# Kernel optimization log

Hardware: AMD Instinct MI355X
Metric: run time of the kernel (lower is better)

The kernel has to match this reference:

```python
import jax, jax.numpy as jnp
import numpy as np

P = 16
IMG_SIZES = [(512, 512), (512, 384), (448, 512), (384, 384), (320, 448), (256, 512), (384, 256), (512, 320)]
LMAX = 1024
B, DIM, HEADS, DH, DEPTH, MLP, NC = 8, 512, 8, 64, 6, 2048, 1000
PD = 3 * P * P  # 768 patch dim


def layer_norm(x, w, b=None, eps=1e-5):
    mu = x.mean(-1, keepdims=True)
    var = ((x - mu) ** 2).mean(-1, keepdims=True)
    y = (x - mu) * jax.lax.rsqrt(var + eps) * w
    return y + b if b is not None else y


def _pack(images):
    # slice each image to its true (static) resolution, patchify, pad to LMAX
    toks, his, wis, msks = [], [], [], []
    for i, (H, W) in enumerate(IMG_SIZES):
        h, w = H // P, W // P
        L = h * w
        img = images[i, :, :H, :W]
        t = img.reshape(3, h, P, w, P).transpose(1, 3, 0, 2, 4).reshape(L, PD)
        hi = jnp.repeat(jnp.arange(h), w)
        wi = jnp.tile(jnp.arange(w), h)
        pad = LMAX - L
        toks.append(jnp.pad(t, ((0, pad), (0, 0))))
        his.append(jnp.pad(hi, (0, pad)))
        wis.append(jnp.pad(wi, (0, pad)))
        msks.append(jnp.arange(LMAX) < L)
    return jnp.stack(toks), jnp.stack(his), jnp.stack(wis), jnp.stack(msks)


def _mha(qx, kx, kmask, wq, wk, wv, qn, kn, wo):
    Bq, Lq, _ = qx.shape
    Lk = kx.shape[1]
    q = (qx @ wq.T).reshape(Bq, Lq, HEADS, DH)
    k = (kx @ wk.T).reshape(Bq, Lk, HEADS, DH)
    v = (kx @ wv.T).reshape(Bq, Lk, HEADS, DH)
    q = layer_norm(q, qn)
    k = layer_norm(k, kn)
    s = jnp.einsum('bqhd,bkhd->bhqk', q, k) / np.sqrt(DH).astype(np.float32)
    s = s + jnp.where(kmask[:, None, None, :], 0.0, -1e9)
    a = jax.nn.softmax(s, axis=-1)
    o = jnp.einsum('bhqk,bkhd->bqhd', a, v).reshape(Bq, Lq, HEADS * DH)
    return o @ wo.T


def setup_inputs() -> dict:
    key = jax.random.key(0)
    ks = iter(jax.random.split(key, 48))

    def nrm(shape, s=0.02):
        return jax.random.normal(next(ks), shape, jnp.float32) * s

    return {
        'images': jax.random.normal(next(ks), (B, 3, 512, 512), jnp.float32),
        'pe_ln1_w': jnp.ones(PD), 'pe_ln1_b': jnp.zeros(PD),
        'pe_w': nrm((DIM, PD)), 'pe_b': jnp.zeros(DIM),
        'pe_ln2_w': jnp.ones(DIM), 'pe_ln2_b': jnp.zeros(DIM),
        'pos_h': nrm((32, DIM), 1.0), 'pos_w': nrm((32, DIM), 1.0),
        'attn_ln': jnp.ones((DEPTH, DIM)),
        'wq': nrm((DEPTH, DIM, DIM)), 'wk': nrm((DEPTH, DIM, DIM)), 'wv': nrm((DEPTH, DIM, DIM)),
        'qn': jnp.ones((DEPTH, DH)), 'kn': jnp.ones((DEPTH, DH)),
        'wo': nrm((DEPTH, DIM, DIM)),
        'ff_ln': jnp.ones((DEPTH, DIM)),
        'ff_w1': nrm((DEPTH, MLP, DIM)), 'ff_b1': jnp.zeros((DEPTH, MLP)),
        'ff_w2': nrm((DEPTH, DIM, MLP)), 'ff_b2': jnp.zeros((DEPTH, DIM)),
        'final_ln': jnp.ones(DIM),
        'pool_q': nrm((DIM,), 1.0), 'pool_ln': jnp.ones(DIM),
        'pool_wq': nrm((DIM, DIM)), 'pool_wk': nrm((DIM, DIM)), 'pool_wv': nrm((DIM, DIM)),
        'pool_qn': jnp.ones(DH), 'pool_kn': jnp.ones(DH),
        'pool_wo': nrm((DIM, DIM)),
        'head_ln': jnp.ones(DIM), 'head_w': nrm((NC, DIM)),
    }


def reference(images, pe_ln1_w, pe_ln1_b, pe_w, pe_b, pe_ln2_w, pe_ln2_b, pos_h, pos_w,
              attn_ln, wq, wk, wv, qn, kn, wo, ff_ln, ff_w1, ff_b1, ff_w2, ff_b2,
              final_ln, pool_q, pool_ln, pool_wq, pool_wk, pool_wv, pool_qn, pool_kn,
              pool_wo, head_ln, head_w):
    tok, hi, wi, mask = _pack(images)
    t = layer_norm(tok, pe_ln1_w, pe_ln1_b)
    t = t @ pe_w.T + pe_b
    t = layer_norm(t, pe_ln2_w, pe_ln2_b)
    t = t + pos_h[hi] + pos_w[wi]
    t = t * mask[..., None]
    for l in range(DEPTH):
        xn = layer_norm(t, attn_ln[l])
        t = t + _mha(xn, xn, mask, wq[l], wk[l], wv[l], qn[l], kn[l], wo[l])
        h = layer_norm(t, ff_ln[l])
        t = t + (jax.nn.gelu(h @ ff_w1[l].T + ff_b1[l], approximate=False) @ ff_w2[l].T + ff_b2[l])
    t = layer_norm(t, final_ln)
    # attention pooling: one learned query per image; context = transformer output (unnormed inside attn)
    q = jnp.broadcast_to(pool_q, (B, 1, DIM))
    qn_ = layer_norm(q, pool_ln)
    pooled = _mha(qn_, t, mask, pool_wq, pool_wk, pool_wv, pool_qn, pool_kn, pool_wo)[:, 0]
    return layer_norm(pooled, head_ln) @ head_w.T
```

## Files before the change

kernel.cpp:

```cpp
#include <hip/hip_runtime.h>
#include <math.h>

#define LMAXS 1024
#define NB 8
#define DIM 512
#define HEADS 8
#define DH 64
#define DEPTH 6
#define MLP 2048
#define NC 1000
#define PDIM 768
#define MPACK 5376
#define MVALID 5360
#define QSCALE 0.18033688f

typedef __attribute__((ext_vector_type(8))) short short8;
typedef __attribute__((ext_vector_type(4))) float floatx4;
typedef unsigned short ushort;

__constant__ int c_w[8]   = {32,24,32,24,28,32,16,20};
__constant__ int c_L[8]   = {1024,768,896,576,560,512,384,640};
__constant__ int c_off[9] = {0,1024,1792,2688,3264,3824,4336,4720,5360};

__device__ __forceinline__ int row2img(int r) {
  int b = 0;
  #pragma unroll
  for (int i = 1; i < 8; ++i) if (r >= c_off[i]) b = i;
  return b;
}

__device__ __forceinline__ ushort f2bf(float x) {
  unsigned int u = __float_as_uint(x);
  u += 0x7fff + ((u >> 16) & 1);
  return (ushort)(u >> 16);
}

#define GLOAD_LDS16(gp, lp) \
  __builtin_amdgcn_global_load_lds((const __attribute__((address_space(1))) void*)(gp), \
                                   (__attribute__((address_space(3))) void*)(lp), 16, 0, 0)

__device__ __forceinline__ void reduce2_256(float& s, float& s2, float* red) {
  #pragma unroll
  for (int off = 32; off; off >>= 1) {
    s  += __shfl_xor(s, off);
    s2 += __shfl_xor(s2, off);
  }
  int wv = threadIdx.x >> 6;
  if ((threadIdx.x & 63) == 0) { red[wv*2] = s; red[wv*2+1] = s2; }
  __syncthreads();
  s  = red[0] + red[2] + red[4] + red[6];
  s2 = red[1] + red[3] + red[5] + red[7];
  __syncthreads();
}

__global__ __launch_bounds__(256) void cvt_k(const float* __restrict__ s, ushort* __restrict__ d, int n) {
  int i = blockIdx.x*256 + threadIdx.x;
  if (i < n) d[i] = f2bf(s[i]);
}
__global__ __launch_bounds__(256) void cvt_qkv_k(
    const float* __restrict__ wq, const float* __restrict__ wk, const float* __restrict__ wv,
    ushort* __restrict__ d) {
  int i = blockIdx.x*256 + threadIdx.x;
  if (i >= 6*1536*512) return;
  int l = i / (1536*512), r = (i / 512) % 1536, k = i & 511;
  const float* src = (r < 512) ? wq : (r < 1024) ? wk : wv;
  int rr = r & 511;
  d[i] = f2bf(src[(size_t)l*DIM*DIM + (size_t)rr*DIM + k]);
}
__global__ __launch_bounds__(256) void cvt_pool_k(
    const float* __restrict__ wk, const float* __restrict__ wv, ushort* __restrict__ d) {
  int i = blockIdx.x*256 + threadIdx.x;
  if (i >= 1024*512) return;
  int r = i >> 9, k = i & 511;
  d[i] = f2bf(r < 512 ? wk[(size_t)r*DIM + k] : wv[(size_t)(r-512)*DIM + k]);
}

__global__ __launch_bounds__(256) void pack_ln1_k(
    const float* __restrict__ images, const float* __restrict__ g,
    const float* __restrict__ bb, ushort* __restrict__ tok) {
  int r = blockIdx.x;
  ushort* out = tok + (size_t)r * PDIM;
  if (r >= MVALID) {
    for (int i = threadIdx.x; i < PDIM; i += 256) out[i] = 0;
    return;
  }
  int b = row2img(r), l = r - c_off[b];
  int wgrid = c_w[b];
  __shared__ float vals[PDIM];
  __shared__ float red[8];
  int hp = l / wgrid, wp = l % wgrid;
  const float* base = images + (size_t)b*3*512*512 + (size_t)hp*16*512 + wp*16;
  float s = 0.f, s2 = 0.f;
  for (int i = threadIdx.x; i < PDIM; i += 256) {
    int c = i >> 8, rr = (i >> 4) & 15, cc = i & 15;
    float v = base[(size_t)c*512*512 + rr*512 + cc];
    vals[i] = v; s += v; s2 += v*v;
  }
  reduce2_256(s, s2, red);
  float mu = s * (1.f/PDIM);
  float rs = rsqrtf(fmaxf(s2*(1.f/PDIM) - mu*mu, 0.f) + 1e-5f);
  for (int i = threadIdx.x; i < PDIM; i += 256)
    out[i] = f2bf((vals[i]-mu)*rs*g[i] + bb[i]);
}

template<int TM, int TN, int WM, int WN, int ACT, int OUT>
__global__ __launch_bounds__(256) void gemm_t(
    const ushort* __restrict__ A, const ushort* __restrict__ W,
    const float* __restrict__ bias, void* __restrict__ Cv,
    int M, int N, int K) {
  constexpr int WAVES_N = TN / WN;
  constexpr int FM = WM / 16, FN = WN / 16;
  constexpr int NA = TM / 32, NW = TN / 32;
  __shared__ ushort As[TM*64];
  __shared__ ushort Ws[TN*64];
  int tid = threadIdx.x;
  int row0 = blockIdx.y*TM, col0 = blockIdx.x*TN;
  int lane = tid & 63, l15 = lane & 15, quad = lane >> 4;
  int wv = tid >> 6;
  int wm = wv / WAVES_N, wn = wv % WAVES_N;
  int sw = l15 & 7;
  int segA = (quad ^ sw) * 8, segB = segA ^ 32;
  const ushort *Ap[NA], *Wp[NW];
  #pragma unroll
  for (int j = 0; j < NA; ++j) {
    int blk = j*256 + tid;
    int r = blk >> 3, s = ((blk & 7) ^ (r & 7)) * 8;
    Ap[j] = A + (size_t)(row0 + r)*K + s;
  }
  #pragma unroll
  for (int j = 0; j < NW; ++j) {
    int blk = j*256 + tid;
    int r = blk >> 3, s = ((blk & 7) ^ (r & 7)) * 8;
    Wp[j] = W + (size_t)(col0 + r)*K + s;
  }
  floatx4 acc[FM][FN] = {};
  for (int k0 = 0; k0 < K; k0 += 64) {
    __syncthreads();
    #pragma unroll
    for (int j = 0; j < NA; ++j) GLOAD_LDS16(Ap[j] + k0, &As[(j*256+tid)*8]);
    #pragma unroll
    for (int j = 0; j < NW; ++j) GLOAD_LDS16(Wp[j] + k0, &Ws[(j*256+tid)*8]);
    __syncthreads();
    #pragma unroll
    for (int w = 0; w < 2; ++w) {
      int sg = w ? segB : segA;
      short8 af[FM], bf[FN];
      #pragma unroll
      for (int i = 0; i < FM; ++i) af[i] = *(const short8*)&As[(wm*WM + i*16 + l15)*64 + sg];
      #pragma unroll
      for (int j = 0; j < FN; ++j) bf[j] = *(const short8*)&Ws[(wn*WN + j*16 + l15)*64 + sg];
      #pragma unroll
      for (int i = 0; i < FM; ++i)
        #pragma unroll
        for (int j = 0; j < FN; ++j)
          acc[i][j] = __builtin_amdgcn_mfma_f32_16x16x32_bf16(af[i], bf[j], acc[i][j], 0, 0, 0);
    }
  }
  int rb = row0 + wm*WM + quad*4;
  int cb = col0 + wn*WN + l15;
  #pragma unroll
  for (int j = 0; j < FN; ++j) {
    int cc = cb + j*16;
    float bsum = bias ? bias[cc] : 0.f;
    #pragma unroll
    for (int i = 0; i < FM; ++i) {
      int rr = rb + i*16;
      #pragma unroll
      for (int reg = 0; reg < 4; ++reg) {
        float v = acc[i][j][reg] + bsum;
        if (ACT == 1) v = 0.5f*v*(1.f + erff(v*0.70710678118654752f));
        size_t idx = (size_t)(rr + reg)*N + cc;
        if (OUT == 0)      ((float*)Cv)[idx] = v;
        else if (OUT == 1) ((float*)Cv)[idx] += v;
        else               ((ushort*)Cv)[idx] = f2bf(v);
      }
    }
  }
}

template<int POOL>
__global__ __launch_bounds__(256) void gemm_qkv_k(
    const ushort* __restrict__ A, const ushort* __restrict__ W,
    const float* __restrict__ gq, const float* __restrict__ gk,
    ushort* __restrict__ Qh, ushort* __restrict__ Kh, ushort* __restrict__ Vh,
    float* __restrict__ KV, int N) {
  const int K = DIM;
  __shared__ ushort As[128*64];
  __shared__ ushort Ws[128*64];
  int tid = threadIdx.x;
  int row0 = blockIdx.y*128, col0 = blockIdx.x*128;
  int lane = tid & 63, l15 = lane & 15, quad = lane >> 4;
  int wv = tid >> 6, wm = wv >> 1, wn = wv & 1;
  int sw = l15 & 7;
  int segA = (quad ^ sw) * 8, segB = segA ^ 32;
  const ushort *Ap[4], *Wp[4];
  #pragma unroll
  for (int j = 0; j < 4; ++j) {
    int blk = j*256 + tid;
    int r = blk >> 3, s = ((blk & 7) ^ (r & 7)) * 8;
    Ap[j] = A + (size_t)(row0 + r)*K + s;
    Wp[j] = W + (size_t)(col0 + r)*K + s;
  }
  floatx4 acc[4][4] = {};
  for (int k0 = 0; k0 < K; k0 += 64) {
    __syncthreads();
    #pragma unroll
    for (int j = 0; j < 4; ++j) {
      GLOAD_LDS16(Ap[j] + k0, &As[(j*256+tid)*8]);
      GLOAD_LDS16(Wp[j] + k0, &Ws[(j*256+tid)*8]);
    }
    __syncthreads();
    #pragma unroll
    for (int w = 0; w < 2; ++w) {
      int sg = w ? segB : segA;
      short8 af[4], bf[4];
      #pragma unroll
      for (int i = 0; i < 4; ++i) af[i] = *(const short8*)&As[(wm*64 + i*16 + l15)*64 + sg];
      #pragma unroll
      for (int j = 0; j < 4; ++j) bf[j] = *(const short8*)&Ws[(wn*64 + j*16 + l15)*64 + sg];
      #pragma unroll
      for (int i = 0; i < 4; ++i)
        #pragma unroll
        for (int j = 0; j < 4; ++j)
          acc[i][j] = __builtin_amdgcn_mfma_f32_16x16x32_bf16(af[i], bf[j], acc[i][j], 0, 0, 0);
    }
  }
  int unit = (col0 >> 6) + wn;
  bool needln = POOL ? (unit < 8) : (unit < 16);
  const float* gain = POOL ? gq : (unit < 8 ? gq : gk);
  #pragma unroll
  for (int i = 0; i < 4; ++i) {
    float s[4] = {0,0,0,0}, s2[4] = {0,0,0,0};
    if (needln) {
      #pragma unroll
      for (int j = 0; j < 4; ++j)
        #pragma unroll
        for (int reg = 0; reg < 4; ++reg) {
          float v = acc[i][j][reg];
          s[reg] += v; s2[reg] += v*v;
        }
      #pragma unroll
      for (int reg = 0; reg < 4; ++reg)
        #pragma unroll
        for (int off = 1; off < 16; off <<= 1) {
          s[reg]  += __shfl_xor(s[reg],  off);
          s2[reg] += __shfl_xor(s2[reg], off);
        }
    }
    #pragma unroll
    for (int reg = 0; reg < 4; ++reg) {
      int r = row0 + wm*64 + i*16 + quad*4 + reg;
      if (r >= MVALID) continue;
      float mu = s[reg]*(1.f/64.f);
      float rs = rsqrtf(fmaxf(s2[reg]*(1.f/64.f) - mu*mu, 0.f) + 1e-5f);
      int b = row2img(r), l = r - c_off[b];
      #pragma unroll
      for (int j = 0; j < 4; ++j) {
        int dh = j*16 + l15;
        float v = acc[i][j][reg];
        if (needln) v = (v - mu)*rs*gain[dh];
        if (POOL) {
          KV[(size_t)r*1024 + unit*64 + dh] = v;
        } else {
          int h = unit & 7;
          size_t dst = ((size_t)(b*8+h)*LMAXS + l)*64 + dh;
          if (unit < 8)       Qh[dst] = f2bf(v * QSCALE);
          else if (unit < 16) Kh[dst] = f2bf(v);
          else                Vh[dst] = f2bf(v);
        }
      }
    }
  }
}

__global__ __launch_bounds__(256) void row_ln_bf_k(
    const float* __restrict__ T, const float* __restrict__ g, ushort* __restrict__ Y) {
  __shared__ float red[8];
  size_t base = (size_t)blockIdx.x * DIM;
  float v0 = T[base + threadIdx.x], v1 = T[base + threadIdx.x + 256];
  float s = v0 + v1, s2 = v0*v0 + v1*v1;
  reduce2_256(s, s2, red);
  float mu = s*(1.f/DIM), rs = rsqrtf(fmaxf(s2*(1.f/DIM) - mu*mu, 0.f) + 1e-5f);
  Y[base + threadIdx.x]       = f2bf((v0-mu)*rs*g[threadIdx.x]);
  Y[base + threadIdx.x + 256] = f2bf((v1-mu)*rs*g[threadIdx.x + 256]);
}

__global__ __launch_bounds__(256) void ln2_pos_k(
    float* __restrict__ T, const float* __restrict__ g, const float* __restrict__ bb,
    const float* __restrict__ ph, const float* __restrict__ pw) {
  int r = blockIdx.x;
  float* x = T + (size_t)r * DIM;
  if (r >= MVALID) {
    for (int i = threadIdx.x; i < DIM; i += 256) x[i] = 0.f;
    return;
  }
  int b = row2img(r), l = r - c_off[b];
  __shared__ float red[8];
  int wgrid = c_w[b];
  int hi = l / wgrid, wi = l % wgrid;
  float s=0.f, s2=0.f;
  for (int i = threadIdx.x; i < DIM; i += 256) { float v = x[i]; s+=v; s2+=v*v; }
  reduce2_256(s, s2, red);
  float mu = s*(1.f/DIM), rs = rsqrtf(fmaxf(s2*(1.f/DIM)-mu*mu, 0.f)+1e-5f);
  for (int i = threadIdx.x; i < DIM; i += 256)
    x[i] = (x[i]-mu)*rs*g[i] + bb[i] + ph[hi*DIM+i] + pw[wi*DIM+i];
}

__global__ __launch_bounds__(256) void vtrans_k(
    const ushort* __restrict__ Vh, ushort* __restrict__ VhT) {
  int bh = blockIdx.x, b = bh >> 3;
  int Lb = c_L[b];
  int lt = blockIdx.y;
  if (lt*64 >= Lb) return;
  __shared__ ushort t[64][72];
  int tid = threadIdx.x;
  int row = tid >> 2, seg = (tid & 3)*16;
  short8 z8 = {};
  if (lt*64 + row < Lb) {
    const ushort* src = Vh + ((size_t)bh*LMAXS + lt*64 + row)*64 + seg;
    *(short8*)&t[row][seg]   = *(const short8*)src;
    *(short8*)&t[row][seg+8] = *(const short8*)(src+8);
  } else {
    *(short8*)&t[row][seg]   = z8;
    *(short8*)&t[row][seg+8] = z8;
  }
  __syncthreads();
  int dh = tid >> 2, ks = (tid & 3)*16;
  short8 o0, o1;
  #pragma unroll
  for (int jj = 0; jj < 8; ++jj) o0[jj] = (short)t[ks+jj][dh];
  #pragma unroll
  for (int jj = 0; jj < 8; ++jj) o1[jj] = (short)t[ks+8+jj][dh];
  ushort* dst = VhT + ((size_t)bh*64 + dh)*LMAXS + lt*64 + ks;
  *(short8*)dst     = o0;
  *(short8*)(dst+8) = o1;
}

__global__ __launch_bounds__(256) void attn_part_k(
    const ushort* __restrict__ Qh, const ushort* __restrict__ Kh,
    const ushort* __restrict__ VhT, float* __restrict__ PART) {
  int bh = blockIdx.x, b = bh >> 3;
  int Lb = c_L[b];
  int qt = blockIdx.y, z = blockIdx.z;
  if (qt*64 >= Lb || z*512 >= Lb) return;
  __shared__ ushort Ks[64*64];
  __shared__ ushort Vt[64*64];
  __shared__ ushort Pb[4][16][68];
  int tid = threadIdx.x, wv = tid >> 6, lane = tid & 63;
  int quad = lane >> 4, l15 = lane & 15;
  int sw = l15 & 7;
  int segA = (quad ^ sw) * 8, segB = segA ^ 32;
  int q0 = qt*64 + wv*16;
  bool active = q0 < Lb;
  const ushort* qhb = Qh + (size_t)bh * LMAXS * DH;
  const ushort* khb = Kh + (size_t)bh * LMAXS * DH;
  const ushort* vtb = VhT + (size_t)bh * DH * LMAXS;
  short8 aq0 = {}, aq1 = {};
  if (active) {
    const ushort* qp = qhb + (size_t)(q0 + l15) * DH;
    aq0 = *(const short8*)(qp + quad*8);
    aq1 = *(const short8*)(qp + 32 + quad*8);
  }
  int blk0 = tid, blk1 = tid + 256;
  int kr0 = blk0 >> 3, s0 = ((blk0 & 7) ^ (kr0 & 7)) * 8;
  int kr1 = blk1 >> 3, s1 = ((blk1 & 7) ^ (kr1 & 7)) * 8;
  const ushort* kg0 = khb + kr0*DH + s0;
  const ushort* kg1 = khb + kr1*DH + s1;
  const ushort* vg0 = vtb + (size_t)kr0*LMAXS + s0;
  const ushort* vg1 = vtb + (size_t)kr1*LMAXS + s1;
  int kbeg = z*512, kend = min(kbeg + 512, Lb);
  float lsum[4] = {0.f,0.f,0.f,0.f};
  floatx4 o[4] = {};
  for (int kc = kbeg; kc < kend; kc += 64) {
    __syncthreads();
    GLOAD_LDS16(kg0 + kc*DH, &Ks[blk0*8]);
    GLOAD_LDS16(kg1 + kc*DH, &Ks[blk1*8]);
    GLOAD_LDS16(vg0 + kc,    &Vt[blk0*8]);
    GLOAD_LDS16(vg1 + kc,    &Vt[blk1*8]);
    __syncthreads();
    if (!active) continue;
    bool tail = (kc + 64 > Lb);
    #pragma unroll
    for (int kb = 0; kb < 4; ++kb) {
      int krow = (kb*16 + l15) * 64;
      floatx4 s = {};
      s = __builtin_amdgcn_mfma_f32_16x16x32_bf16(aq0, *(const short8*)&Ks[krow + segA], s, 0,0,0);
      s = __builtin_amdgcn_mfma_f32_16x16x32_bf16(aq1, *(const short8*)&Ks[krow + segB], s, 0,0,0);
      #pragma unroll
      for (int reg = 0; reg < 4; ++reg) {
        float x = s[reg];
        if (tail && (kc + kb*16 + l15 >= Lb)) x = -1e9f;
        float p = __builtin_amdgcn_exp2f(x);
        lsum[reg] += p;
        Pb[wv][quad*4+reg][kb*16+l15] = f2bf(p);
      }
    }
    short8 a0 = *(const short8*)&Pb[wv][l15][quad*8];
    short8 a1 = *(const short8*)&Pb[wv][l15][32+quad*8];
    #pragma unroll
    for (int nb = 0; nb < 4; ++nb) {
      int vrow = (nb*16 + l15) * 64;
      o[nb] = __builtin_amdgcn_mfma_f32_16x16x32_bf16(a0, *(const short8*)&Vt[vrow + segA], o[nb], 0,0,0);
      o[nb] = __builtin_amdgcn_mfma_f32_16x16x32_bf16(a1, *(const short8*)&Vt[vrow + segB], o[nb], 0,0,0);
    }
  }
  if (active) {
    size_t sb = ((size_t)(bh*16 + qt)*2 + z) * 4160;
    #pragma unroll
    for (int reg = 0; reg < 4; ++reg) {
      float s = lsum[reg];
      s += __shfl_xor(s,1); s += __shfl_xor(s,2); s += __shfl_xor(s,4); s += __shfl_xor(s,8);
      if (l15 == 0) PART[sb + 4096 + wv*16 + quad*4 + reg] = s;
    }
    int rq = wv*16 + quad*4;
    #pragma unroll
    for (int nb = 0; nb < 4; ++nb)
      #pragma unroll
      for (int reg = 0; reg < 4; ++reg)
        PART[sb + (size_t)(rq + reg)*64 + nb*16 + l15] = o[nb][reg];
  }
}

__global__ __launch_bounds__(256) void attn_comb_k(
    const float* __restrict__ PART, ushort* __restrict__ O) {
  int bh = blockIdx.x, b = bh >> 3, h = bh & 7;
  int Lb = c_L[b];
  int qt = blockIdx.y;
  if (qt*64 >= Lb) return;
  int nsl = (Lb + 511) >> 9;
  int t = threadIdx.x;
  int q = t >> 2, dj = (t & 3) * 16;
  int qq = qt*64 + q;
  if (qq >= Lb) return;
  size_t base = (size_t)(bh*16 + qt)*2*4160;
  float o[16] = {};
  float l = 0.f;
  for (int zz = 0; zz < nsl; ++zz) {
    const float* sp = PART + base + (size_t)zz*4160;
    #pragma unroll
    for (int i = 0; i < 16; i += 4) {
      float4 v = *(const float4*)&sp[q*64 + dj + i];
      o[i] += v.x; o[i+1] += v.y; o[i+2] += v.z; o[i+3] += v.w;
    }
    l += sp[4096 + q];
  }
  float inv = 1.f / l;
  short8 r0, r1;
  #pragma unroll
  for (int i = 0; i < 8; ++i) r0[i] = (short)f2bf(o[i]*inv);
  #pragma unroll
  for (int i = 0; i < 8; ++i) r1[i] = (short)f2bf(o[8+i]*inv);
  ushort* dst = O + (size_t)(c_off[b]+qq)*DIM + h*DH + dj;
  *(short8*)dst     = r0;
  *(short8*)(dst+8) = r1;
}

__global__ __launch_bounds__(256) void pool_prep_a_k(
    const float* __restrict__ pq, const float* __restrict__ pln,
    const float* __restrict__ pwq, float* __restrict__ qp) {
  __shared__ float qln[DIM];
  __shared__ float red[8];
  int tid = threadIdx.x;
  float s=0.f, s2=0.f;
  for (int i=tid;i<DIM;i+=256){ float v=pq[i]; s+=v; s2+=v*v; }
  reduce2_256(s, s2, red);
  float mu=s*(1.f/DIM), rs=rsqrtf(fmaxf(s2*(1.f/DIM)-mu*mu,0.f)+1e-5f);
  for (int i=tid;i<DIM;i+=256) qln[i]=(pq[i]-mu)*rs*pln[i];
  __syncthreads();
  int n = blockIdx.x*64 + (tid>>2);
  int kq = (tid&3)*128;
  const float4* wr = (const float4*)(pwq + (size_t)n*DIM + kq);
  float a=0.f;
  #pragma unroll
  for (int k=0;k<32;++k) {
    float4 w4 = wr[k];
    float4 q4 = *(const float4*)&qln[kq + k*4];
    a += w4.x*q4.x + w4.y*q4.y + w4.z*q4.z + w4.w*q4.w;
  }
  a += __shfl_xor(a,1); a += __shfl_xor(a,2);
  if ((tid&3)==0) qp[n]=a;
}

__global__ __launch_bounds__(512) void pool_prep_b_k(
    const float* __restrict__ qp, const float* __restrict__ pqn, float* __restrict__ qpool) {
  int h = threadIdx.x >> 6, lane = threadIdx.x & 63;
  float v = qp[h*64 + lane];
  float s = v, s2 = v*v;
  #pragma unroll
  for (int off=32; off; off>>=1) { s += __shfl_xor(s,off); s2 += __shfl_xor(s2,off); }
  float mu = s*(1.f/64), rs = rsqrtf(fmaxf(s2*(1.f/64)-mu*mu, 0.f)+1e-5f);
  qpool[h*64+lane] = (v-mu)*rs*pqn[lane];
}

__global__ __launch_bounds__(256) void pool_attn_part_k(
    const float* __restrict__ qpool, const float* __restrict__ KV,
    float* __restrict__ PARTP) {
  __shared__ float qh[DH];
  __shared__ float ps[256];
  __shared__ float op[4][DH];
  __shared__ float red[8];
  int bh = blockIdx.x, c = blockIdx.y;
  int b = bh>>3, h = bh&7;
  int Lb = c_L[b];
  int tid = threadIdx.x;
  if (tid < DH) qh[tid] = qpool[h*DH + tid];
  __syncthreads();
  int kk = c*256 + tid;
  float p = 0.f;
  if (kk < Lb) {
    const float4* kp = (const float4*)(KV + (size_t)(c_off[b]+kk)*1024 + h*DH);
    float a = 0.f;
    #pragma unroll
    for (int dd=0; dd<16; ++dd) {
      float4 kv = kp[dd];
      a += kv.x*qh[dd*4] + kv.y*qh[dd*4+1] + kv.z*qh[dd*4+2] + kv.w*qh[dd*4+3];
    }
    p = __expf(a*0.125f);
  }
  ps[tid] = p;
  float s = p, s2 = 0.f;
  reduce2_256(s, s2, red);
  int wvv = tid >> 6, lane = tid & 63;
  float o = 0.f;
  int kb = c*256 + wvv*64;
  const float* vb = KV + (size_t)c_off[b]*1024 + 512 + h*DH + lane;
  for (int j = 0; j < 64; ++j) {
    int key = kb + j;
    if (key < Lb) o += ps[wvv*64+j] * vb[(size_t)key*1024];
  }
  op[wvv][lane] = o;
  __syncthreads();
  if (tid < DH)
    PARTP[((size_t)bh*4 + c)*66 + tid] = op[0][tid]+op[1][tid]+op[2][tid]+op[3][tid];
  if (tid == 64)
    PARTP[((size_t)bh*4 + c)*66 + 64] = s;
}

__global__ __launch_bounds__(64) void pool_attn_comb_k(
    const float* __restrict__ PARTP, float* __restrict__ O) {
  int bh = blockIdx.x, b = bh>>3, h = bh&7, d = threadIdx.x;
  float o = 0.f, sum = 0.f;
  #pragma unroll
  for (int c = 0; c < 4; ++c) {
    o   += PARTP[((size_t)bh*4 + c)*66 + d];
    sum += PARTP[((size_t)bh*4 + c)*66 + 64];
  }
  O[(size_t)b*DIM + h*DH + d] = o / sum;
}

__global__ __launch_bounds__(256) void proj512_k(
    const float* __restrict__ X, const float* __restrict__ W, float* __restrict__ Y) {
  __shared__ float xr[DIM];
  int b = blockIdx.x, tid = threadIdx.x;
  for (int i=tid;i<DIM;i+=256) xr[i] = X[(size_t)b*DIM+i];
  __syncthreads();
  if (tid < 128) {
    int n = blockIdx.y*128 + tid;
    const float4* wr = (const float4*)(W + (size_t)n*DIM);
    float a=0.f;
    for (int k=0;k<DIM/4;++k) { float4 w4 = wr[k]; a += w4.x*xr[k*4]+w4.y*xr[k*4+1]+w4.z*xr[k*4+2]+w4.w*xr[k*4+3]; }
    Y[(size_t)b*DIM+n]=a;
  }
}

__global__ __launch_bounds__(256) void head_out_k(
    const float* __restrict__ X, const float* __restrict__ g,
    const float* __restrict__ W, float* __restrict__ out) {
  __shared__ float xr[DIM];
  __shared__ float red[8];
  int b = blockIdx.x, tid = threadIdx.x;
  float s=0.f, s2=0.f;
  for (int i=tid;i<DIM;i+=256){ float v=X[(size_t)b*DIM+i]; s+=v; s2+=v*v; }
  reduce2_256(s, s2, red);
  float mu=s*(1.f/DIM), rs=rsqrtf(fmaxf(s2*(1.f/DIM)-mu*mu,0.f)+1e-5f);
  for (int i=tid;i<DIM;i+=256) xr[i]=(X[(size_t)b*DIM+i]-mu)*rs*g[i];
  __syncthreads();
  if (tid < 125) {
    int n = blockIdx.y*125 + tid;
    const float4* wr = (const float4*)(W + (size_t)n*DIM);
    float a=0.f;
    for (int k=0;k<DIM/4;++k){ float4 w4=wr[k]; a += w4.x*xr[k*4]+w4.y*xr[k*4+1]+w4.z*xr[k*4+2]+w4.w*xr[k*4+3]; }
    out[(size_t)b*NC+n]=a;
  }
}

extern "C" void kernel_launch(void* const* d_in, const int* in_sizes, int n_in,
                              void* d_out, int out_size, void* d_ws, size_t ws_size,
                              hipStream_t stream) {
  const float* images  = (const float*)d_in[0];
  const float* pe_ln1_w= (const float*)d_in[1];
  const float* pe_ln1_b= (const float*)d_in[2];
  const float* pe_w    = (const float*)d_in[3];
  const float* pe_b    = (const float*)d_in[4];
  const float* pe_ln2_w= (const float*)d_in[5];
  const float* pe_ln2_b= (const float*)d_in[6];
  const float* pos_h   = (const float*)d_in[7];
  const float* pos_w   = (const float*)d_in[8];
  const float* attn_ln = (const float*)d_in[9];
  const float* wq      = (const float*)d_in[10];
  const float* wk      = (const float*)d_in[11];
  const float* wvp     = (const float*)d_in[12];
  const float* qn      = (const float*)d_in[13];
  const float* kn      = (const float*)d_in[14];
  const float* wo      = (const float*)d_in[15];
  const float* ff_ln   = (const float*)d_in[16];
  const float* ff_w1   = (const float*)d_in[17];
  const float* ff_b1   = (const float*)d_in[18];
  const float* ff_w2   = (const float*)d_in[19];
  const float* ff_b2   = (const float*)d_in[20];
  const float* final_ln= (const float*)d_in[21];
  const float* pool_q  = (const float*)d_in[22];
  const float* pool_ln = (const float*)d_in[23];
  const float* pool_wq = (const float*)d_in[24];
  const float* pool_wk = (const float*)d_in[25];
  const float* pool_wv = (const float*)d_in[26];
  const float* pool_qn = (const float*)d_in[27];
  const float* pool_kn = (const float*)d_in[28];
  const float* pool_wo = (const float*)d_in[29];
  const float* head_ln = (const float*)d_in[30];
  const float* head_w  = (const float*)d_in[31];
  (void)ws_size; (void)in_sizes; (void)n_in; (void)out_size;

  char* p = (char*)d_ws;
  ushort* WQKVc = (ushort*)p; p += (size_t)6*1536*512*2;
  ushort* WOc   = (ushort*)p; p += (size_t)6*512*512*2;
  ushort* W1c   = (ushort*)p; p += (size_t)6*2048*512*2;
  ushort* W2c   = (ushort*)p; p += (size_t)6*512*2048*2;
  ushort* PEWc  = (ushort*)p; p += (size_t)512*768*2;
  ushort* PKVc  = (ushort*)p; p += (size_t)1024*512*2;
  float*  T     = (float*)p;  p += (size_t)MPACK*DIM*4;
  ushort* XN    = (ushort*)p; p += (size_t)MPACK*DIM*2;
  ushort* Qh    = (ushort*)p; p += (size_t)64*LMAXS*DH*2;
  ushort* Kh    = (ushort*)p; p += (size_t)64*LMAXS*DH*2;
  ushort* Vh    = (ushort*)p; p += (size_t)64*LMAXS*DH*2;
  ushort* VhT   = (ushort*)p; p += (size_t)64*64*LMAXS*2;
  ushort* FFH   = (ushort*)p; p += (size_t)MPACK*MLP*2;
  ushort* TOK   = FFH;
  ushort* ATTO  = FFH;
  float*  PART  = (float*)p;  p += (size_t)64*16*2*4160*4;
  float*  KVb   = (float*)p;  p += (size_t)MPACK*1024*4;
  float*  QP    = (float*)p;  p += DIM*4;
  float*  QPOOL = (float*)p;  p += DIM*4;
  float*  POOLO = (float*)p;  p += NB*DIM*4;
  float*  POOLED= (float*)p;  p += NB*DIM*4;
  float*  PARTP = (float*)p;  p += (size_t)64*4*66*4;

  cvt_qkv_k<<<(6*1536*512+255)/256, 256, 0, stream>>>(wq, wk, wvp, WQKVc);
  cvt_k<<<(6*512*512+255)/256, 256, 0, stream>>>(wo, WOc, 6*512*512);
  cvt_k<<<(6*2048*512+255)/256, 256, 0, stream>>>(ff_w1, W1c, 6*2048*512);
  cvt_k<<<(6*512*2048+255)/256, 256, 0, stream>>>(ff_w2, W2c, 6*512*2048);
  cvt_k<<<(512*768+255)/256, 256, 0, stream>>>(pe_w, PEWc, 512*768);
  cvt_pool_k<<<(1024*512+255)/256, 256, 0, stream>>>(pool_wk, pool_wv, PKVc);

  pack_ln1_k<<<MPACK, 256, 0, stream>>>(images, pe_ln1_w, pe_ln1_b, TOK);
  gemm_t<64,128,64,32,0,0><<<dim3(4, MPACK/64), 256, 0, stream>>>(TOK, PEWc, pe_b, T, MPACK, DIM, PDIM);
  ln2_pos_k<<<MPACK, 256, 0, stream>>>(T, pe_ln2_w, pe_ln2_b, pos_h, pos_w);

  for (int l = 0; l < DEPTH; ++l) {
    row_ln_bf_k<<<MPACK, 256, 0, stream>>>(T, attn_ln + l*DIM, XN);
    gemm_qkv_k<0><<<dim3(12, MPACK/128), 256, 0, stream>>>(
        XN, WQKVc + (size_t)l*1536*512, qn + l*DH, kn + l*DH, Qh, Kh, Vh, nullptr, 1536);
    vtrans_k<<<dim3(64, 16), 256, 0, stream>>>(Vh, VhT);
    attn_part_k<<<dim3(64, 16, 2), 256, 0, stream>>>(Qh, Kh, VhT, PART);
    attn_comb_k<<<dim3(64, 16), 256, 0, stream>>>(PART, ATTO);
    gemm_t<64,64,32,32,0,1><<<dim3(8, MPACK/64), 256, 0, stream>>>(ATTO, WOc + (size_t)l*512*512, nullptr, T, MPACK, DIM, DIM);
    row_ln_bf_k<<<MPACK, 256, 0, stream>>>(T, ff_ln + l*DIM, XN);
    gemm_t<64,128,64,32,1,2><<<dim3(16, MPACK/64), 256, 0, stream>>>(XN, W1c + (size_t)l*MLP*DIM, ff_b1 + l*MLP, FFH, MPACK, MLP, DIM);
    gemm_t<64,64,32,32,0,1><<<dim3(8, MPACK/64), 256, 0, stream>>>(FFH, W2c + (size_t)l*DIM*MLP, ff_b2 + l*DIM, T, MPACK, DIM, MLP);
  }

  row_ln_bf_k<<<MPACK, 256, 0, stream>>>(T, final_ln, XN);
  pool_prep_a_k<<<8, 256, 0, stream>>>(pool_q, pool_ln, pool_wq, QP);
  pool_prep_b_k<<<1, 512, 0, stream>>>(QP, pool_qn, QPOOL);
  gemm_qkv_k<1><<<dim3(8, MPACK/128), 256, 0, stream>>>(
      XN, PKVc, pool_kn, nullptr, nullptr, nullptr, nullptr, KVb, 1024);
  pool_attn_part_k<<<dim3(64, 4), 256, 0, stream>>>(QPOOL, KVb, PARTP);
  pool_attn_comb_k<<<64, 64, 0, stream>>>(PARTP, POOLO);
  proj512_k<<<dim3(8, 4), 256, 0, stream>>>(POOLO, pool_wo, POOLED);
  head_out_k<<<dim3(8, 8), 256, 0, stream>>>(POOLED, head_ln, head_w, (float*)d_out);
}
```

Measured before the change: 1.240 ms.

## Fuse V transpose into QKV epilogue and merge weight-conversion and pool-prep kernels

The QKV GEMM epilogue now writes V straight into the transposed [bh][dh][L] layout. This removes the separate vtrans kernel and the Vh intermediate buffer every layer. The six weight-conversion launches become one kernel that converts four floats per thread, and the two pooling-query prep kernels become a single 512-thread kernel. The transposed V stores are strided 2-byte writes that coalesce poorly. Padding columns in VhT past each image's length are no longer zeroed, which could matter if attention reads them.

```diff
diff --git a/kernel.cpp b/kernel.cpp
--- a/kernel.cpp
+++ b/kernel.cpp
@@ -53,26 +53,39 @@
   __syncthreads();
 }
 
-__global__ __launch_bounds__(256) void cvt_k(const float* __restrict__ s, ushort* __restrict__ d, int n) {
-  int i = blockIdx.x*256 + threadIdx.x;
-  if (i < n) d[i] = f2bf(s[i]);
-}
-__global__ __launch_bounds__(256) void cvt_qkv_k(
+__global__ __launch_bounds__(256) void cvt_all_k(
     const float* __restrict__ wq, const float* __restrict__ wk, const float* __restrict__ wv,
-    ushort* __restrict__ d) {
-  int i = blockIdx.x*256 + threadIdx.x;
-  if (i >= 6*1536*512) return;
-  int l = i / (1536*512), r = (i / 512) % 1536, k = i & 511;
-  const float* src = (r < 512) ? wq : (r < 1024) ? wk : wv;
-  int rr = r & 511;
-  d[i] = f2bf(src[(size_t)l*DIM*DIM + (size_t)rr*DIM + k]);
-}
-__global__ __launch_bounds__(256) void cvt_pool_k(
-    const float* __restrict__ wk, const float* __restrict__ wv, ushort* __restrict__ d) {
-  int i = blockIdx.x*256 + threadIdx.x;
-  if (i >= 1024*512) return;
-  int r = i >> 9, k = i & 511;
-  d[i] = f2bf(r < 512 ? wk[(size_t)r*DIM + k] : wv[(size_t)(r-512)*DIM + k]);
+    const float* __restrict__ wo, const float* __restrict__ w1, const float* __restrict__ w2,
+    const float* __restrict__ pew, const float* __restrict__ pwk, const float* __restrict__ pwv,
+    ushort* __restrict__ WQKV, ushort* __restrict__ WO, ushort* __restrict__ W1,
+    ushort* __restrict__ W2, ushort* __restrict__ PEW, ushort* __restrict__ PKV) {
+  const long N0 = 4718592L;
+  const long N1 = N0 + 1572864L;
+  const long N2 = N1 + 6291456L;
+  const long N3 = N2 + 6291456L;
+  const long N4 = N3 + 393216L;
+  const long N5 = N4 + 524288L;
+  long e = ((long)blockIdx.x*256 + threadIdx.x) * 4;
+  if (e >= N5) return;
+  const float* src; ushort* dst;
+  if (e < N0) {
+    long i = e;
+    int l = (int)(i / (1536L*512)); int r = (int)((i/512) % 1536); int k = (int)(i & 511);
+    const float* s = (r < 512) ? wq : (r < 1024) ? wk : wv;
+    int rr = r & 511;
+    src = s + (size_t)l*DIM*DIM + (size_t)rr*DIM + k; dst = WQKV + i;
+  } else if (e < N1) { long o = e-N0; src = wo  + o; dst = WO  + o; }
+  else if (e < N2)   { long o = e-N1; src = w1  + o; dst = W1  + o; }
+  else if (e < N3)   { long o = e-N2; src = w2  + o; dst = W2  + o; }
+  else if (e < N4)   { long o = e-N3; src = pew + o; dst = PEW + o; }
+  else {
+    long i = e-N4; int r = (int)(i >> 9); int k = (int)(i & 511);
+    src = (r < 512) ? (pwk + (size_t)r*DIM + k) : (pwv + (size_t)(r-512)*DIM + k);
+    dst = PKV + i;
+  }
+  float4 v = *(const float4*)src;
+  ushort4 o4; o4.x=f2bf(v.x); o4.y=f2bf(v.y); o4.z=f2bf(v.z); o4.w=f2bf(v.w);
+  *(ushort4*)dst = o4;
 }
 
 __global__ __launch_bounds__(256) void pack_ln1_k(
@@ -182,7 +195,7 @@
 __global__ __launch_bounds__(256) void gemm_qkv_k(
     const ushort* __restrict__ A, const ushort* __restrict__ W,
     const float* __restrict__ gq, const float* __restrict__ gk,
-    ushort* __restrict__ Qh, ushort* __restrict__ Kh, ushort* __restrict__ Vh,
+    ushort* __restrict__ Qh, ushort* __restrict__ Kh, ushort* __restrict__ VhT,
     float* __restrict__ KV, int N) {
   const int K = DIM;
   __shared__ ushort As[128*64];
@@ -263,10 +276,13 @@
           KV[(size_t)r*1024 + unit*64 + dh] = v;
         } else {
           int h = unit & 7;
-          size_t dst = ((size_t)(b*8+h)*LMAXS + l)*64 + dh;
-          if (unit < 8)       Qh[dst] = f2bf(v * QSCALE);
-          else if (unit < 16) Kh[dst] = f2bf(v);
-          else                Vh[dst] = f2bf(v);
+          if (unit < 8) {
+            Qh[((size_t)(b*8+h)*LMAXS + l)*64 + dh] = f2bf(v * QSCALE);
+          } else if (unit < 16) {
+            Kh[((size_t)(b*8+h)*LMAXS + l)*64 + dh] = f2bf(v);
+          } else {
+            VhT[((size_t)(b*8+h)*64 + dh)*LMAXS + l] = f2bf(v);
+          }
         }
       }
     }
@@ -304,36 +320,6 @@
   float mu = s*(1.f/DIM), rs = rsqrtf(fmaxf(s2*(1.f/DIM)-mu*mu, 0.f)+1e-5f);
   for (int i = threadIdx.x; i < DIM; i += 256)
     x[i] = (x[i]-mu)*rs*g[i] + bb[i] + ph[hi*DIM+i] + pw[wi*DIM+i];
-}
-
-__global__ __launch_bounds__(256) void vtrans_k(
-    const ushort* __restrict__ Vh, ushort* __restrict__ VhT) {
-  int bh = blockIdx.x, b = bh >> 3;
-  int Lb = c_L[b];
-  int lt = blockIdx.y;
-  if (lt*64 >= Lb) return;
-  __shared__ ushort t[64][72];
-  int tid = threadIdx.x;
-  int row = tid >> 2, seg = (tid & 3)*16;
-  short8 z8 = {};
-  if (lt*64 + row < Lb) {
-    const ushort* src = Vh + ((size_t)bh*LMAXS + lt*64 + row)*64 + seg;
-    *(short8*)&t[row][seg]   = *(const short8*)src;
-    *(short8*)&t[row][seg+8] = *(const short8*)(src+8);
-  } else {
-    *(short8*)&t[row][seg]   = z8;
-    *(short8*)&t[row][seg+8] = z8;
-  }
-  __syncthreads();
-  int dh = tid >> 2, ks = (tid & 3)*16;
-  short8 o0, o1;
-  #pragma unroll
-  for (int jj = 0; jj < 8; ++jj) o0[jj] = (short)t[ks+jj][dh];
-  #pragma unroll
-  for (int jj = 0; jj < 8; ++jj) o1[jj] = (short)t[ks+8+jj][dh];
-  ushort* dst = VhT + ((size_t)bh*64 + dh)*LMAXS + lt*64 + ks;
-  *(short8*)dst     = o0;
-  *(short8*)(dst+8) = o1;
 }
 
 __global__ __launch_bounds__(256) void attn_part_k(
@@ -455,41 +441,39 @@
   *(short8*)(dst+8) = r1;
 }
 
-__global__ __launch_bounds__(256) void pool_prep_a_k(
+__global__ __launch_bounds__(512) void pool_prep_k(
     const float* __restrict__ pq, const float* __restrict__ pln,
-    const float* __restrict__ pwq, float* __restrict__ qp) {
+    const float* __restrict__ pwq, const float* __restrict__ pqn,
+    float* __restrict__ qpool) {
   __shared__ float qln[DIM];
-  __shared__ float red[8];
+  __shared__ float red[16];
   int tid = threadIdx.x;
-  float s=0.f, s2=0.f;
-  for (int i=tid;i<DIM;i+=256){ float v=pq[i]; s+=v; s2+=v*v; }
-  reduce2_256(s, s2, red);
-  float mu=s*(1.f/DIM), rs=rsqrtf(fmaxf(s2*(1.f/DIM)-mu*mu,0.f)+1e-5f);
-  for (int i=tid;i<DIM;i+=256) qln[i]=(pq[i]-mu)*rs*pln[i];
-  __syncthreads();
-  int n = blockIdx.x*64 + (tid>>2);
-  int kq = (tid&3)*128;
-  const float4* wr = (const float4*)(pwq + (size_t)n*DIM + kq);
-  float a=0.f;
-  #pragma unroll
-  for (int k=0;k<32;++k) {
+  float v = pq[tid];
+  float s = v, s2 = v*v;
+  #pragma unroll
+  for (int off = 32; off; off >>= 1) { s += __shfl_xor(s, off); s2 += __shfl_xor(s2, off); }
+  int wvv = tid >> 6;
+  if ((tid & 63) == 0) { red[wvv*2] = s; red[wvv*2+1] = s2; }
+  __syncthreads();
+  s = 0.f; s2 = 0.f;
+  #pragma unroll
+  for (int i = 0; i < 8; ++i) { s += red[i*2]; s2 += red[i*2+1]; }
+  float mu = s*(1.f/DIM), rs = rsqrtf(fmaxf(s2*(1.f/DIM)-mu*mu, 0.f)+1e-5f);
+  qln[tid] = (v-mu)*rs*pln[tid];
+  __syncthreads();
+  const float4* wr = (const float4*)(pwq + (size_t)tid*DIM);
+  float a = 0.f;
+  #pragma unroll 8
+  for (int k = 0; k < DIM/4; ++k) {
     float4 w4 = wr[k];
-    float4 q4 = *(const float4*)&qln[kq + k*4];
+    float4 q4 = *(const float4*)&qln[k*4];
     a += w4.x*q4.x + w4.y*q4.y + w4.z*q4.z + w4.w*q4.w;
   }
-  a += __shfl_xor(a,1); a += __shfl_xor(a,2);
-  if ((tid&3)==0) qp[n]=a;
-}
-
-__global__ __launch_bounds__(512) void pool_prep_b_k(
-    const float* __restrict__ qp, const float* __restrict__ pqn, float* __restrict__ qpool) {
-  int h = threadIdx.x >> 6, lane = threadIdx.x & 63;
-  float v = qp[h*64 + lane];
-  float s = v, s2 = v*v;
-  #pragma unroll
-  for (int off=32; off; off>>=1) { s += __shfl_xor(s,off); s2 += __shfl_xor(s2,off); }
-  float mu = s*(1.f/64), rs = rsqrtf(fmaxf(s2*(1.f/64)-mu*mu, 0.f)+1e-5f);
-  qpool[h*64+lane] = (v-mu)*rs*pqn[lane];
+  float hs = a, hs2 = a*a;
+  #pragma unroll
+  for (int off = 32; off; off >>= 1) { hs += __shfl_xor(hs, off); hs2 += __shfl_xor(hs2, off); }
+  float hmu = hs*(1.f/64), hrs = rsqrtf(fmaxf(hs2*(1.f/64)-hmu*hmu, 0.f)+1e-5f);
+  qpool[tid] = (a-hmu)*hrs*pqn[tid & 63];
 }
 
 __global__ __launch_bounds__(256) void pool_attn_part_k(
@@ -632,25 +616,20 @@
   ushort* XN    = (ushort*)p; p += (size_t)MPACK*DIM*2;
   ushort* Qh    = (ushort*)p; p += (size_t)64*LMAXS*DH*2;
   ushort* Kh    = (ushort*)p; p += (size_t)64*LMAXS*DH*2;
-  ushort* Vh    = (ushort*)p; p += (size_t)64*LMAXS*DH*2;
   ushort* VhT   = (ushort*)p; p += (size_t)64*64*LMAXS*2;
   ushort* FFH   = (ushort*)p; p += (size_t)MPACK*MLP*2;
   ushort* TOK   = FFH;
   ushort* ATTO  = FFH;
   float*  PART  = (float*)p;  p += (size_t)64*16*2*4160*4;
   float*  KVb   = (float*)p;  p += (size_t)MPACK*1024*4;
-  float*  QP    = (float*)p;  p += DIM*4;
   float*  QPOOL = (float*)p;  p += DIM*4;
   float*  POOLO = (float*)p;  p += NB*DIM*4;
   float*  POOLED= (float*)p;  p += NB*DIM*4;
   float*  PARTP = (float*)p;  p += (size_t)64*4*66*4;
 
-  cvt_qkv_k<<<(6*1536*512+255)/256, 256, 0, stream>>>(wq, wk, wvp, WQKVc);
-  cvt_k<<<(6*512*512+255)/256, 256, 0, stream>>>(wo, WOc, 6*512*512);
-  cvt_k<<<(6*2048*512+255)/256, 256, 0, stream>>>(ff_w1, W1c, 6*2048*512);
-  cvt_k<<<(6*512*2048+255)/256, 256, 0, stream>>>(ff_w2, W2c, 6*512*2048);
-  cvt_k<<<(512*768+255)/256, 256, 0, stream>>>(pe_w, PEWc, 512*768);
-  cvt_pool_k<<<(1024*512+255)/256, 256, 0, stream>>>(pool_wk, pool_wv, PKVc);
+  cvt_all_k<<<19328, 256, 0, stream>>>(wq, wk, wvp, wo, ff_w1, ff_w2, pe_w,
+                                       pool_wk, pool_wv,
+                                       WQKVc, WOc, W1c, W2c, PEWc, PKVc);
 
   pack_ln1_k<<<MPACK, 256, 0, stream>>>(images, pe_ln1_w, pe_ln1_b, TOK);
   gemm_t<64,128,64,32,0,0><<<dim3(4, MPACK/64), 256, 0, stream>>>(TOK, PEWc, pe_b, T, MPACK, DIM, PDIM);
@@ -659,8 +638,7 @@
   for (int l = 0; l < DEPTH; ++l) {
     row_ln_bf_k<<<MPACK, 256, 0, stream>>>(T, attn_ln + l*DIM, XN);
     gemm_qkv_k<0><<<dim3(12, MPACK/128), 256, 0, stream>>>(
-        XN, WQKVc + (size_t)l*1536*512, qn + l*DH, kn + l*DH, Qh, Kh, Vh, nullptr, 1536);
-    vtrans_k<<<dim3(64, 16), 256, 0, stream>>>(Vh, VhT);
+        XN, WQKVc + (size_t)l*1536*512, qn + l*DH, kn + l*DH, Qh, Kh, VhT, nullptr, 1536);
     attn_part_k<<<dim3(64, 16, 2), 256, 0, stream>>>(Qh, Kh, VhT, PART);
     attn_comb_k<<<dim3(64, 16), 256, 0, stream>>>(PART, ATTO);
     gemm_t<64,64,32,32,0,1><<<dim3(8, MPACK/64), 256, 0, stream>>>(ATTO, WOc + (size_t)l*512*512, nullptr, T, MPACK, DIM, DIM);
@@ -670,8 +648,7 @@
   }
 
   row_ln_bf_k<<<MPACK, 256, 0, stream>>>(T, final_ln, XN);
-  pool_prep_a_k<<<8, 256, 0, stream>>>(pool_q, pool_ln, pool_wq, QP);
-  pool_prep_b_k<<<1, 512, 0, stream>>>(QP, pool_qn, QPOOL);
+  pool_prep_k<<<1, 512, 0, stream>>>(pool_q, pool_ln, pool_wq, pool_qn, QPOOL);
   gemm_qkv_k<1><<<dim3(8, MPACK/128), 256, 0, stream>>>(
       XN, PKVc, pool_kn, nullptr, nullptr, nullptr, nullptr, KVb, 1024);
   pool_attn_part_k<<<dim3(64, 4), 256, 0, stream>>>(QPOOL, KVb, PARTP);
```

Result: no change. 1.263 ms (+1.8%).
